# Kernel tuning notes

Hardware: AMD Instinct MI355X
Metric: run time of the kernel (lower is better)

The kernel has to match this reference:

```python
import jax, jax.numpy as jnp
import numpy as np

K = 1024
HEADS = 16


def setup_inputs() -> dict:
    key = jax.random.key(0)
    ks = jax.random.split(key, 6)
    x = jax.random.normal(ks[0], (2, 2048, K), dtype=jnp.float32)
    sc = 1.0 / np.sqrt(K)
    Wq = jax.random.normal(ks[1], (K, K), dtype=jnp.float32) * sc
    Wk = jax.random.normal(ks[2], (K, K), dtype=jnp.float32) * sc
    Wv = jax.random.normal(ks[3], (K, K), dtype=jnp.float32) * sc
    Wu = jax.random.normal(ks[4], (K, K), dtype=jnp.float32) * sc
    bu = jax.random.normal(ks[5], (K,), dtype=jnp.float32) * 0.01
    return {"x": x, "Wq": Wq, "Wk": Wk, "Wv": Wv, "Wu": Wu, "bu": bu}


def reference(x, Wq, Wk, Wv, Wu, bu):
    b, t, k = x.shape
    h = HEADS
    s = k // h
    # torch Linear: y = x @ W.T
    q = (x @ Wq.T).reshape(b, t, h, s)
    kk = (x @ Wk.T).reshape(b, t, h, s)
    v = (x @ Wv.T).reshape(b, t, h, s)
    # NOTE: original scales by sqrt(k) (full model dim), not sqrt(head dim)
    dot = jnp.einsum('bqhs,bkhs->bhqk', q, kk) / jnp.sqrt(jnp.float32(k))
    attn = jax.nn.softmax(dot, axis=-1)
    out = jnp.einsum('bhqk,bkhs->bqhs', attn, v).reshape(b, t, k)
    return out @ Wu.T + bu
```

## Files before the change

### kernel.cpp

```cpp
#include <hip/hip_runtime.h>
#include <hip/hip_bf16.h>


typedef __bf16 bf16x8 __attribute__((ext_vector_type(8)));
typedef float f32x4 __attribute__((ext_vector_type(4)));
typedef float f32x16 __attribute__((ext_vector_type(16)));
typedef unsigned int u32x4 __attribute__((ext_vector_type(4)));

static __device__ __forceinline__ unsigned short f2bf(float f) {
  union { float f; unsigned u; } a; a.f = f;
  unsigned r = a.u + 0x7fff + ((a.u >> 16) & 1);
  return (unsigned short)(r >> 16);
}

static __device__ __forceinline__ unsigned cvt_pk_bf16(float lo, float hi) {
  unsigned r;
  asm("v_cvt_pk_bf16_f32 %0, %1, %2" : "=v"(r) : "v"(lo), "v"(hi));
  return r;
}

static __device__ __forceinline__ float fexp2(float x) {
#if __has_builtin(__builtin_amdgcn_exp2f)
  return __builtin_amdgcn_exp2f(x);
#else
  float r; asm("v_exp_f32 %0, %1\n\ts_nop 0" : "=v"(r) : "v"(x)); return r;
#endif
}

static __device__ __forceinline__ void swap32(unsigned a, unsigned b,
                                              unsigned& x, unsigned& y, int hi) {
#if __has_builtin(__builtin_amdgcn_permlane32_swap)
  typedef unsigned u32x2 __attribute__((ext_vector_type(2)));
  u32x2 r = __builtin_amdgcn_permlane32_swap(a, b, false, false);
  x = r.x; y = r.y;
#else
  unsigned pa = (unsigned)__shfl_xor((int)a, 32, 64);
  unsigned pb = (unsigned)__shfl_xor((int)b, 32, 64);
  x = hi ? pb : a;
  y = hi ? b : pa;
#endif
}

static __device__ __forceinline__ void gload_lds16(const unsigned short* g, unsigned short* l) {
  __builtin_amdgcn_global_load_lds((const __attribute__((address_space(1))) void*)g,
                                   (__attribute__((address_space(3))) void*)l, 16, 0, 0);
}

static __device__ __forceinline__ float tsum16(const f32x16& v) {
  float a0 = v[0]+v[1], a1 = v[2]+v[3], a2 = v[4]+v[5], a3 = v[6]+v[7];
  float a4 = v[8]+v[9], a5 = v[10]+v[11], a6 = v[12]+v[13], a7 = v[14]+v[15];
  float b0 = a0+a1, b1 = a2+a3, b2 = a4+a5, b3 = a6+a7;
  return (b0+b1) + (b2+b3);
}

__global__ __launch_bounds__(256)
void cast_all(const float* __restrict__ x, const float* __restrict__ wq,
              const float* __restrict__ wk, const float* __restrict__ wv,
              const float* __restrict__ wu,
              unsigned short* __restrict__ xb, unsigned short* __restrict__ wqb,
              unsigned short* __restrict__ wkb, unsigned short* __restrict__ wvb,
              unsigned short* __restrict__ wub)
{
  int bid = blockIdx.x;
  const float* src; unsigned short* dst; int blk;
  if (bid < 4096)      { src = x;  dst = xb;  blk = bid; }
  else if (bid < 5120) { src = wq; dst = wqb; blk = bid - 4096; }
  else if (bid < 6144) { src = wk; dst = wkb; blk = bid - 5120; }
  else if (bid < 7168) { src = wv; dst = wvb; blk = bid - 6144; }
  else                 { src = wu; dst = wub; blk = bid - 7168; }
  int idx = blk * 1024 + threadIdx.x * 4;
  float4 v = *(const float4*)&src[idx];
  ushort4 o;
  o.x = f2bf(v.x); o.y = f2bf(v.y); o.z = f2bf(v.z); o.w = f2bf(v.w);
  *(ushort4*)&dst[idx] = o;
}

__global__ __launch_bounds__(512, 2)
void gemm_qkv(const unsigned short* __restrict__ A,
              const unsigned short* __restrict__ Bq,
              const unsigned short* __restrict__ Bk,
              const unsigned short* __restrict__ Bv,
              unsigned short* __restrict__ Qo,
              unsigned short* __restrict__ Ko,
              unsigned short* __restrict__ Vo)
{
  const int Ksz = 1024;
  __shared__ __align__(16) unsigned short As[2][128 * 32];
  __shared__ __align__(16) unsigned short Bs[2][128 * 32];
  const int z = blockIdx.z;
  const unsigned short* B = (z == 0) ? Bq : (z == 1) ? Bk : Bv;
  const int tid  = threadIdx.x;
  const int lane = tid & 63;
  const int wid  = tid >> 6;
  const int wr   = wid >> 2, wc = wid & 3;
  const int g    = lane >> 4, r = lane & 15;
  const int bm   = blockIdx.x * 128, bn = blockIdx.y * 128;

  f32x4 acc[4][2] = {};

  const int grow = lane >> 2;
  const int gcol = (lane & 3) * 8;
  const unsigned short* Ag = &A[(size_t)(bm + wid*16 + grow) * Ksz + gcol];
  const unsigned short* Bg = &B[(size_t)(bn + wid*16 + grow) * Ksz + gcol];

  gload_lds16(Ag, &As[0][wid * 512]);
  gload_lds16(Bg, &Bs[0][wid * 512]);
  __syncthreads();

  int buf = 0;
  for (int k0 = 0; k0 < Ksz; k0 += 32) {
    if (k0 + 32 < Ksz) {
      gload_lds16(Ag + k0 + 32, &As[buf^1][wid * 512]);
      gload_lds16(Bg + k0 + 32, &Bs[buf^1][wid * 512]);
    }
    bf16x8 af[4], bfr[2];
#pragma unroll
    for (int mi = 0; mi < 4; ++mi)
      af[mi] = *(const bf16x8*)&As[buf][(wr*64 + mi*16 + r) * 32 + g*8];
#pragma unroll
    for (int ni = 0; ni < 2; ++ni)
      bfr[ni] = *(const bf16x8*)&Bs[buf][(wc*32 + ni*16 + r) * 32 + g*8];
#pragma unroll
    for (int mi = 0; mi < 4; ++mi)
#pragma unroll
      for (int ni = 0; ni < 2; ++ni)
        acc[mi][ni] = __builtin_amdgcn_mfma_f32_16x16x32_bf16(af[mi], bfr[ni], acc[mi][ni], 0, 0, 0);
    __syncthreads();
    buf ^= 1;
  }

  const float scale = (z == 0) ? (0.03125f * 1.4426950408889634f) : 1.0f;
#pragma unroll
  for (int mi = 0; mi < 4; ++mi)
#pragma unroll
    for (int ni = 0; ni < 2; ++ni) {
      if (z == 2) {
        int m0 = bm + wr*64 + mi*16 + g*4;
        int n  = bn + wc*32 + ni*16 + r;
        int b = m0 >> 11, t0 = m0 & 2047;
        int h = n >> 6,  s = n & 63;
        ushort4 o;
        o.x = f2bf(acc[mi][ni][0]); o.y = f2bf(acc[mi][ni][1]);
        o.z = f2bf(acc[mi][ni][2]); o.w = f2bf(acc[mi][ni][3]);
        *(ushort4*)&Vo[((size_t)((b*16 + h)*64 + s)) * 2048 + t0] = o;
      } else {
        unsigned short* dst = (z == 0) ? Qo : Ko;
#pragma unroll
        for (int q = 0; q < 4; ++q) {
          int m = bm + wr*64 + mi*16 + g*4 + q;
          int n = bn + wc*32 + ni*16 + r;
          int b = m >> 11, t = m & 2047;
          int h = n >> 6,  s = n & 63;
          dst[((size_t)((b*16 + h)*2048 + t)) * 64 + s] = f2bf(acc[mi][ni][q] * scale);
        }
      }
    }
}

__global__ __launch_bounds__(512, 2)
void gemm_final(const unsigned short* __restrict__ A,
                const unsigned short* __restrict__ B,
                float* __restrict__ Cf,
                const float* __restrict__ bias)
{
  const int Ksz = 1024, N = 1024;
  __shared__ __align__(16) unsigned short As[2][128 * 32];
  __shared__ __align__(16) unsigned short Bs[2][128 * 32];
  const int tid  = threadIdx.x;
  const int lane = tid & 63;
  const int wid  = tid >> 6;
  const int wr   = wid >> 2, wc = wid & 3;
  const int g    = lane >> 4, r = lane & 15;
  const int bm   = blockIdx.x * 128, bn = blockIdx.y * 128;

  f32x4 acc[4][2] = {};

  const int grow = lane >> 2;
  const int gcol = (lane & 3) * 8;
  const unsigned short* Ag = &A[(size_t)(bm + wid*16 + grow) * Ksz + gcol];
  const unsigned short* Bg = &B[(size_t)(bn + wid*16 + grow) * Ksz + gcol];

  gload_lds16(Ag, &As[0][wid * 512]);
  gload_lds16(Bg, &Bs[0][wid * 512]);
  __syncthreads();

  int buf = 0;
  for (int k0 = 0; k0 < Ksz; k0 += 32) {
    if (k0 + 32 < Ksz) {
      gload_lds16(Ag + k0 + 32, &As[buf^1][wid * 512]);
      gload_lds16(Bg + k0 + 32, &Bs[buf^1][wid * 512]);
    }
    bf16x8 af[4], bfr[2];
#pragma unroll
    for (int mi = 0; mi < 4; ++mi)
      af[mi] = *(const bf16x8*)&As[buf][(wr*64 + mi*16 + r) * 32 + g*8];
#pragma unroll
    for (int ni = 0; ni < 2; ++ni)
      bfr[ni] = *(const bf16x8*)&Bs[buf][(wc*32 + ni*16 + r) * 32 + g*8];
#pragma unroll
    for (int mi = 0; mi < 4; ++mi)
#pragma unroll
      for (int ni = 0; ni < 2; ++ni)
        acc[mi][ni] = __builtin_amdgcn_mfma_f32_16x16x32_bf16(af[mi], bfr[ni], acc[mi][ni], 0, 0, 0);
    __syncthreads();
    buf ^= 1;
  }

#pragma unroll
  for (int mi = 0; mi < 4; ++mi)
#pragma unroll
    for (int ni = 0; ni < 2; ++ni)
#pragma unroll
      for (int q = 0; q < 4; ++q) {
        int m = bm + wr*64 + mi*16 + g*4 + q;
        int n = bn + wc*32 + ni*16 + r;
        Cf[(size_t)m * N + n] = acc[mi][ni][q] + bias[n];
      }
}

__global__ __launch_bounds__(256)
void attn_kernel(const unsigned short* __restrict__ Qg,
                 const unsigned short* __restrict__ Kg,
                 const unsigned short* __restrict__ Vtg,
                 unsigned short* __restrict__ Og)
{
  const int T = 2048;
  __shared__ __align__(16) unsigned short sK[2][128 * 64];
  __shared__ __align__(16) unsigned short sV[2][64 * 128];

  const int tid = threadIdx.x, lane = tid & 63, wid = tid >> 6;
  const int q32 = lane & 31;
  const int kh  = lane >> 5;

  int bid  = blockIdx.x + 16 * blockIdx.y;
  int nb   = (bid & 7) * 64 + (bid >> 3);
  int bh   = nb >> 4;
  int qblk = nb & 15;
  int qbase = qblk * 128 + wid * 32;

  const size_t base = (size_t)bh * T * 64;
  const unsigned short* Qh = Qg + base;
  const unsigned short* Kh = Kg + base;
  const unsigned short* Vh = Vtg + base;

  const int krow_l  = lane >> 3;
  const int kchunk  = (lane & 7) ^ (krow_l & 7);
  const int vrow_l  = lane >> 4;
  const int vchunkp = lane & 15;

  bf16x8 qf[4];
#pragma unroll
  for (int s = 0; s < 4; ++s)
    qf[s] = *(const bf16x8*)&Qh[(size_t)(qbase + q32)*64 + s*16 + kh*8];

  f32x16 oacc[2] = {};
  float l_own = 0.f;

#pragma unroll
  for (int r = 0; r < 4; ++r) {
    int kr = r*32 + wid*8;
    gload_lds16(Kh + (size_t)(kr + krow_l)*64 + kchunk*8, &sK[0][kr*64]);
    int vr = r*16 + wid*4;
    int vrow = vr + vrow_l;
    gload_lds16(Vh + (size_t)vrow*T + ((vchunkp ^ (vrow & 7))*8), &sV[0][vr*128]);
  }
  __syncthreads();

  int buf = 0;
#pragma unroll 1
  for (int t = 0; t < 16; ++t) {
    if (t < 15) {
      const int kv1 = (t + 1) * 128;
#pragma unroll
      for (int r = 0; r < 4; ++r) {
        int kr = r*32 + wid*8;
        gload_lds16(Kh + (size_t)(kv1 + kr + krow_l)*64 + kchunk*8,
                    &sK[buf^1][kr*64]);
        int vr = r*16 + wid*4;
        int vrow = vr + vrow_l;
        gload_lds16(Vh + (size_t)vrow*T + kv1 + ((vchunkp ^ (vrow & 7))*8),
                    &sV[buf^1][vr*128]);
      }
    }

#pragma unroll
    for (int st = 0; st < 4; ++st) {
      f32x16 a = {};
      const int kvr = st*32 + q32;
#pragma unroll
      for (int s = 0; s < 4; ++s) {
        const int c = (s*2 + kh) ^ (kvr & 7);
        bf16x8 kf = *(const bf16x8*)&sK[buf][kvr*64 + c*8];
        a = __builtin_amdgcn_mfma_f32_32x32x16_bf16(kf, qf[s], a, 0, 0, 0);
      }
#pragma unroll
      for (int r = 0; r < 16; ++r)
        a[r] = fexp2(a[r]);
      l_own += tsum16(a);

      unsigned U[8];
#pragma unroll
      for (int i = 0; i < 8; ++i)
        U[i] = cvt_pk_bf16(a[2*i], a[2*i + 1]);
      unsigned w[8];
      swap32(U[0], U[2], w[0], w[2], kh);
      swap32(U[1], U[3], w[1], w[3], kh);
      swap32(U[4], U[6], w[4], w[6], kh);
      swap32(U[5], U[7], w[5], w[7], kh);
#pragma unroll
      for (int c = 0; c < 2; ++c) {
        u32x4 pw = { w[c*4 + 0], w[c*4 + 1], w[c*4 + 2], w[c*4 + 3] };
        bf16x8 pf = __builtin_bit_cast(bf16x8, pw);
#pragma unroll
        for (int mt = 0; mt < 2; ++mt) {
          const int sr = mt*32 + q32;
          const int cc = (st*4 + c*2 + kh) ^ (sr & 7);
          bf16x8 vfr = *(const bf16x8*)&sV[buf][sr*128 + cc*8];
          oacc[mt] = __builtin_amdgcn_mfma_f32_32x32x16_bf16(vfr, pf, oacc[mt], 0, 0, 0);
        }
      }
    }

    __syncthreads();
    buf ^= 1;
  }

  const float l = l_own + __shfl_xor(l_own, 32, 64);
  const int h = bh & 15, b = bh >> 4;
  const float inv = 1.0f / l;
  const int tq = qbase + q32;
#pragma unroll
  for (int mt = 0; mt < 2; ++mt)
#pragma unroll
    for (int rg = 0; rg < 4; ++rg) {
      ushort4 o;
      o.x = f2bf(oacc[mt][rg*4 + 0] * inv);
      o.y = f2bf(oacc[mt][rg*4 + 1] * inv);
      o.z = f2bf(oacc[mt][rg*4 + 2] * inv);
      o.w = f2bf(oacc[mt][rg*4 + 3] * inv);
      int sd = mt*32 + rg*8 + kh*4;
      *(ushort4*)&Og[((size_t)(b*2048 + tq))*1024 + h*64 + sd] = o;
    }
}

extern "C" void kernel_launch(void* const* d_in, const int* in_sizes, int n_in,
                              void* d_out, int out_size, void* d_ws, size_t ws_size,
                              hipStream_t stream) {
  const float* x  = (const float*)d_in[0];
  const float* Wq = (const float*)d_in[1];
  const float* Wk = (const float*)d_in[2];
  const float* Wv = (const float*)d_in[3];
  const float* Wu = (const float*)d_in[4];
  const float* bu = (const float*)d_in[5];
  float* out = (float*)d_out;

  char* ws = (char*)d_ws;
  unsigned short* xb  = (unsigned short*)(ws);
  unsigned short* Wqb = (unsigned short*)(ws + (size_t)( 8<<20));
  unsigned short* Wkb = (unsigned short*)(ws + (size_t)(10<<20));
  unsigned short* Wvb = (unsigned short*)(ws + (size_t)(12<<20));
  unsigned short* Wub = (unsigned short*)(ws + (size_t)(14<<20));
  unsigned short* Qg  = (unsigned short*)(ws + (size_t)(16<<20));
  unsigned short* Kg  = (unsigned short*)(ws + (size_t)(24<<20));
  unsigned short* Vtg = (unsigned short*)(ws + (size_t)(32<<20));
  unsigned short* Ab  = xb;

  cast_all<<<dim3(8192), 256, 0, stream>>>(x, Wq, Wk, Wv, Wu, xb, Wqb, Wkb, Wvb, Wub);

  gemm_qkv<<<dim3(32, 8, 3), 512, 0, stream>>>(xb, Wqb, Wkb, Wvb, Qg, Kg, Vtg);

  attn_kernel<<<dim3(16, 32), 256, 0, stream>>>(Qg, Kg, Vtg, Ab);

  gemm_final<<<dim3(32, 8), 512, 0, stream>>>(Ab, Wub, out, bu);
}
```

Baseline: 114.8 us.

## Double GEMM K-tile to 64 and XOR-swizzle LDS layout

Both projection GEMMs now stage 64-wide K slices per iteration instead of 32, halving the number of barrier-separated iterations, and each lane issues two global-to-LDS loads per operand. The LDS layout uses an XOR swizzle on 16-byte chunks (chunk ^ row&7), applied on both the global load addressing and the fragment reads, to avoid bank conflicts when reading 128-byte rows. LDS use per block doubles to 64KB, which may limit the two-blocks-per-CU occupancy target.

```diff
diff --git a/kernel.cpp b/kernel.cpp
--- a/kernel.cpp
+++ b/kernel.cpp
@@ -85,8 +85,8 @@
               unsigned short* __restrict__ Vo)
 {
   const int Ksz = 1024;
-  __shared__ __align__(16) unsigned short As[2][128 * 32];
-  __shared__ __align__(16) unsigned short Bs[2][128 * 32];
+  __shared__ __align__(16) unsigned short As[2][128 * 64];
+  __shared__ __align__(16) unsigned short Bs[2][128 * 64];
   const int z = blockIdx.z;
   const unsigned short* B = (z == 0) ? Bq : (z == 1) ? Bk : Bv;
   const int tid  = threadIdx.x;
@@ -98,33 +98,48 @@
 
   f32x4 acc[4][2] = {};
 
-  const int grow = lane >> 2;
-  const int gcol = (lane & 3) * 8;
-  const unsigned short* Ag = &A[(size_t)(bm + wid*16 + grow) * Ksz + gcol];
-  const unsigned short* Bg = &B[(size_t)(bn + wid*16 + grow) * Ksz + gcol];
-
-  gload_lds16(Ag, &As[0][wid * 512]);
-  gload_lds16(Bg, &Bs[0][wid * 512]);
+  const int srow   = lane >> 3;
+  const int schunk = (lane & 7) ^ srow;
+  const unsigned short* Ag0 = &A[(size_t)(bm + wid*16 +     srow) * Ksz + schunk*8];
+  const unsigned short* Ag1 = &A[(size_t)(bm + wid*16 + 8 + srow) * Ksz + schunk*8];
+  const unsigned short* Bg0 = &B[(size_t)(bn + wid*16 +     srow) * Ksz + schunk*8];
+  const unsigned short* Bg1 = &B[(size_t)(bn + wid*16 + 8 + srow) * Ksz + schunk*8];
+
+  gload_lds16(Ag0, &As[0][(wid*16    ) * 64]);
+  gload_lds16(Ag1, &As[0][(wid*16 + 8) * 64]);
+  gload_lds16(Bg0, &Bs[0][(wid*16    ) * 64]);
+  gload_lds16(Bg1, &Bs[0][(wid*16 + 8) * 64]);
   __syncthreads();
 
   int buf = 0;
-  for (int k0 = 0; k0 < Ksz; k0 += 32) {
-    if (k0 + 32 < Ksz) {
-      gload_lds16(Ag + k0 + 32, &As[buf^1][wid * 512]);
-      gload_lds16(Bg + k0 + 32, &Bs[buf^1][wid * 512]);
-    }
-    bf16x8 af[4], bfr[2];
-#pragma unroll
-    for (int mi = 0; mi < 4; ++mi)
-      af[mi] = *(const bf16x8*)&As[buf][(wr*64 + mi*16 + r) * 32 + g*8];
-#pragma unroll
-    for (int ni = 0; ni < 2; ++ni)
-      bfr[ni] = *(const bf16x8*)&Bs[buf][(wc*32 + ni*16 + r) * 32 + g*8];
-#pragma unroll
-    for (int mi = 0; mi < 4; ++mi)
-#pragma unroll
-      for (int ni = 0; ni < 2; ++ni)
-        acc[mi][ni] = __builtin_amdgcn_mfma_f32_16x16x32_bf16(af[mi], bfr[ni], acc[mi][ni], 0, 0, 0);
+  for (int k0 = 0; k0 < Ksz; k0 += 64) {
+    if (k0 + 64 < Ksz) {
+      gload_lds16(Ag0 + k0 + 64, &As[buf^1][(wid*16    ) * 64]);
+      gload_lds16(Ag1 + k0 + 64, &As[buf^1][(wid*16 + 8) * 64]);
+      gload_lds16(Bg0 + k0 + 64, &Bs[buf^1][(wid*16    ) * 64]);
+      gload_lds16(Bg1 + k0 + 64, &Bs[buf^1][(wid*16 + 8) * 64]);
+    }
+#pragma unroll
+    for (int kk = 0; kk < 2; ++kk) {
+      bf16x8 af[4], bfr[2];
+#pragma unroll
+      for (int mi = 0; mi < 4; ++mi) {
+        int row = wr*64 + mi*16 + r;
+        int c = (g + kk*4) ^ (row & 7);
+        af[mi] = *(const bf16x8*)&As[buf][row*64 + c*8];
+      }
+#pragma unroll
+      for (int ni = 0; ni < 2; ++ni) {
+        int row = wc*32 + ni*16 + r;
+        int c = (g + kk*4) ^ (row & 7);
+        bfr[ni] = *(const bf16x8*)&Bs[buf][row*64 + c*8];
+      }
+#pragma unroll
+      for (int mi = 0; mi < 4; ++mi)
+#pragma unroll
+        for (int ni = 0; ni < 2; ++ni)
+          acc[mi][ni] = __builtin_amdgcn_mfma_f32_16x16x32_bf16(af[mi], bfr[ni], acc[mi][ni], 0, 0, 0);
+    }
     __syncthreads();
     buf ^= 1;
   }
@@ -164,8 +179,8 @@
                 const float* __restrict__ bias)
 {
   const int Ksz = 1024, N = 1024;
-  __shared__ __align__(16) unsigned short As[2][128 * 32];
-  __shared__ __align__(16) unsigned short Bs[2][128 * 32];
+  __shared__ __align__(16) unsigned short As[2][128 * 64];
+  __shared__ __align__(16) unsigned short Bs[2][128 * 64];
   const int tid  = threadIdx.x;
   const int lane = tid & 63;
   const int wid  = tid >> 6;
@@ -175,33 +190,48 @@
 
   f32x4 acc[4][2] = {};
 
-  const int grow = lane >> 2;
-  const int gcol = (lane & 3) * 8;
-  const unsigned short* Ag = &A[(size_t)(bm + wid*16 + grow) * Ksz + gcol];
-  const unsigned short* Bg = &B[(size_t)(bn + wid*16 + grow) * Ksz + gcol];
-
-  gload_lds16(Ag, &As[0][wid * 512]);
-  gload_lds16(Bg, &Bs[0][wid * 512]);
+  const int srow   = lane >> 3;
+  const int schunk = (lane & 7) ^ srow;
+  const unsigned short* Ag0 = &A[(size_t)(bm + wid*16 +     srow) * Ksz + schunk*8];
+  const unsigned short* Ag1 = &A[(size_t)(bm + wid*16 + 8 + srow) * Ksz + schunk*8];
+  const unsigned short* Bg0 = &B[(size_t)(bn + wid*16 +     srow) * Ksz + schunk*8];
+  const unsigned short* Bg1 = &B[(size_t)(bn + wid*16 + 8 + srow) * Ksz + schunk*8];
+
+  gload_lds16(Ag0, &As[0][(wid*16    ) * 64]);
+  gload_lds16(Ag1, &As[0][(wid*16 + 8) * 64]);
+  gload_lds16(Bg0, &Bs[0][(wid*16    ) * 64]);
+  gload_lds16(Bg1, &Bs[0][(wid*16 + 8) * 64]);
   __syncthreads();
 
   int buf = 0;
-  for (int k0 = 0; k0 < Ksz; k0 += 32) {
-    if (k0 + 32 < Ksz) {
-      gload_lds16(Ag + k0 + 32, &As[buf^1][wid * 512]);
-      gload_lds16(Bg + k0 + 32, &Bs[buf^1][wid * 512]);
-    }
-    bf16x8 af[4], bfr[2];
-#pragma unroll
-    for (int mi = 0; mi < 4; ++mi)
-      af[mi] = *(const bf16x8*)&As[buf][(wr*64 + mi*16 + r) * 32 + g*8];
-#pragma unroll
-    for (int ni = 0; ni < 2; ++ni)
-      bfr[ni] = *(const bf16x8*)&Bs[buf][(wc*32 + ni*16 + r) * 32 + g*8];
-#pragma unroll
-    for (int mi = 0; mi < 4; ++mi)
-#pragma unroll
-      for (int ni = 0; ni < 2; ++ni)
-        acc[mi][ni] = __builtin_amdgcn_mfma_f32_16x16x32_bf16(af[mi], bfr[ni], acc[mi][ni], 0, 0, 0);
+  for (int k0 = 0; k0 < Ksz; k0 += 64) {
+    if (k0 + 64 < Ksz) {
+      gload_lds16(Ag0 + k0 + 64, &As[buf^1][(wid*16    ) * 64]);
+      gload_lds16(Ag1 + k0 + 64, &As[buf^1][(wid*16 + 8) * 64]);
+      gload_lds16(Bg0 + k0 + 64, &Bs[buf^1][(wid*16    ) * 64]);
+      gload_lds16(Bg1 + k0 + 64, &Bs[buf^1][(wid*16 + 8) * 64]);
+    }
+#pragma unroll
+    for (int kk = 0; kk < 2; ++kk) {
+      bf16x8 af[4], bfr[2];
+#pragma unroll
+      for (int mi = 0; mi < 4; ++mi) {
+        int row = wr*64 + mi*16 + r;
+        int c = (g + kk*4) ^ (row & 7);
+        af[mi] = *(const bf16x8*)&As[buf][row*64 + c*8];
+      }
+#pragma unroll
+      for (int ni = 0; ni < 2; ++ni) {
+        int row = wc*32 + ni*16 + r;
+        int c = (g + kk*4) ^ (row & 7);
+        bfr[ni] = *(const bf16x8*)&Bs[buf][row*64 + c*8];
+      }
+#pragma unroll
+      for (int mi = 0; mi < 4; ++mi)
+#pragma unroll
+        for (int ni = 0; ni < 2; ++ni)
+          acc[mi][ni] = __builtin_amdgcn_mfma_f32_16x16x32_bf16(af[mi], bfr[ni], acc[mi][ni], 0, 0, 0);
+    }
     __syncthreads();
     buf ^= 1;
   }
```

New measurement: 114.9 us. About the same (+0.1%).
